# Kernel tuning notes

Hardware: AMD Instinct MI355X
Metric: run time of the kernel (lower is better)

The kernel has to match this reference:

```python
import jax, jax.numpy as jnp
import numpy as np

B = 65536
IN = 32 * 8      # input_size * n_dim
H = 256          # joint_hidden_size


def setup_inputs() -> dict:
    key = jax.random.key(0)
    ks = jax.random.split(key, 8)
    joint_h = jax.random.normal(ks[0], (B, H), dtype=jnp.float32)
    mgn_h = jax.random.normal(ks[1], (B, IN), dtype=jnp.float32)
    # xavier-uniform scale for W, plain normal for U (orthogonal in torch; any
    # dense matrix is fine for a numerical reference), zeros for biases.
    w_lim = float(np.sqrt(6.0 / (IN + H)))
    W_r = jax.random.uniform(ks[2], (IN, H), jnp.float32, -w_lim, w_lim)
    W_z = jax.random.uniform(ks[3], (IN, H), jnp.float32, -w_lim, w_lim)
    W_h = jax.random.uniform(ks[4], (IN, H), jnp.float32, -w_lim, w_lim)
    U_r = jax.random.normal(ks[5], (H, H), jnp.float32) / np.float32(np.sqrt(H))
    U_z = jax.random.normal(ks[6], (H, H), jnp.float32) / np.float32(np.sqrt(H))
    U_h = jax.random.normal(ks[7], (H, H), jnp.float32) / np.float32(np.sqrt(H))
    b_r = jnp.zeros((H,), jnp.float32)
    b_z = jnp.zeros((H,), jnp.float32)
    b_h = jnp.zeros((H,), jnp.float32)
    return {"joint_h": joint_h, "mgn_h": mgn_h,
            "W_r": W_r, "W_z": W_z, "W_h": W_h,
            "U_r": U_r, "U_z": U_z, "U_h": U_h,
            "b_r": b_r, "b_z": b_z, "b_h": b_h}


def reference(joint_h, mgn_h, W_r, W_z, W_h, U_r, U_z, U_h, b_r, b_z, b_h):
    # fuse the three input GEMMs and the two non-gated hidden GEMMs by
    # concatenating weights (same math as 6 separate mm's)
    W = jnp.concatenate([W_r, W_z, W_h], axis=1)        # [IN, 3H]
    U_rz = jnp.concatenate([U_r, U_z], axis=1)          # [H, 2H]
    x_proj = mgn_h @ W                                  # [B, 3H]
    h_proj = joint_h @ U_rz                             # [B, 2H]
    Hd = joint_h.shape[1]
    r = jax.nn.sigmoid(x_proj[:, :Hd] + h_proj[:, :Hd] + b_r)
    z = jax.nn.sigmoid(x_proj[:, Hd:2 * Hd] + h_proj[:, Hd:] + b_z)
    h_tilde = jnp.tanh(x_proj[:, 2 * Hd:] + (joint_h * r) @ U_h + b_h)
    return h_tilde + z * (joint_h - h_tilde)
```

## Files before the change

kernel.cpp:

```cpp
#include <hip/hip_runtime.h>

#define H     256
#define BM    128
#define NTHR  512
#define LDK2  264

typedef __attribute__((ext_vector_type(4)))  float f32x4;
typedef __attribute__((ext_vector_type(16))) float f32x16;
typedef __attribute__((ext_vector_type(8)))  short bf16x8;

__device__ __forceinline__ ushort f2bf(float f) {
    union { float f; unsigned u; } v; v.f = f;
    unsigned u = v.u;
    unsigned r = (u + 0x7fffu + ((u >> 16) & 1u)) >> 16;
    return (ushort)r;
}
__device__ __forceinline__ float bf2f(ushort h) {
    union { unsigned u; float f; } v; v.u = ((unsigned)h) << 16;
    return v.f;
}
__device__ __forceinline__ float sigmoid_f(float x) {
    return __builtin_amdgcn_rcpf(1.0f + __expf(-x));
}
__device__ __forceinline__ float tanh_f(float x) {
    float ax = fabsf(x);
    float e  = __expf(-2.0f * ax);
    float t  = (1.0f - e) * __builtin_amdgcn_rcpf(1.0f + e);
    return copysignf(t, x);
}

__global__ void prep_w(const float* __restrict__ Wr, const float* __restrict__ Wz,
                       const float* __restrict__ Wh, const float* __restrict__ Ur,
                       const float* __restrict__ Uz, const float* __restrict__ Uh,
                       ushort* __restrict__ P)
{
    const int k  = blockIdx.x;
    const int kk = k & 255;
    const bool hi = k >= 256;
    for (int n = threadIdx.x; n < 768; n += 256) {
        float v;
        if (n < 256)      v = (hi ? Ur : Wr)[kk * 256 + n];
        else if (n < 512) v = (hi ? Uz : Wz)[kk * 256 + (n - 256)];
        else              v = (hi ? Uh : Wh)[kk * 256 + (n - 512)];
        P[(size_t)n * 512 + k] = f2bf(v);
    }
}

#define MFMA32(a, b, c) __builtin_amdgcn_mfma_f32_32x32x16_bf16((a), (b), (c), 0, 0, 0)

#define LBRZ(B, BR, BZ) do {                                                  \
    const int ko_ = ((B) < 16) ? (B) * 16 : 256 + ((B) - 16) * 16;            \
    BR = *(const bf16x8*)(pBr + ko_);                                         \
    BZ = *(const bf16x8*)(pBz + ko_);                                         \
} while (0)

#define LBH(B, BH) do {                                                       \
    const int ko_ = ((B) < 16) ? 256 + (B) * 16 : ((B) - 16) * 16;            \
    BH = *(const bf16x8*)(pBh + ko_);                                         \
} while (0)

#define STEP1(SB, S16, BR, BZ) do {                                           \
    const int kk_ = (S16) * 16;                                               \
    bf16x8 af_[4];                                                            \
    _Pragma("unroll") for (int rf_ = 0; rf_ < 4; ++rf_)                       \
        af_[rf_] = *(const bf16x8*)&SB[(rf_ * 32 + l31) * LDK2 + kk_ + hi8];  \
    _Pragma("unroll") for (int rf_ = 0; rf_ < 4; ++rf_) {                     \
        aR[rf_] = MFMA32(af_[rf_], BR, aR[rf_]);                              \
        aZ[rf_] = MFMA32(af_[rf_], BZ, aZ[rf_]);                              \
    }                                                                         \
} while (0)

#define STEP2(SB, S16, BH) do {                                               \
    const int kk_ = (S16) * 16;                                               \
    bf16x8 af_[4];                                                            \
    _Pragma("unroll") for (int rf_ = 0; rf_ < 4; ++rf_)                       \
        af_[rf_] = *(const bf16x8*)&SB[(rf_ * 32 + l31) * LDK2 + kk_ + hi8];  \
    _Pragma("unroll") for (int rf_ = 0; rf_ < 4; ++rf_)                       \
        aH[rf_] = MFMA32(af_[rf_], BH, aH[rf_]);                              \
} while (0)

#define LOADJ(C) do {                                                         \
    _Pragma("unroll") for (int i_ = 0; i_ < 4; ++i_) {                        \
        const int c_ = tid + ((C) * 4 + i_) * NTHR;                           \
        jv[i_] = *(const f32x4*)(joint + (r0 + (c_ >> 6)) * H + (c_ & 63) * 4); \
    }                                                                         \
} while (0)

#define COMMITJ(C) do {                                                       \
    _Pragma("unroll") for (int i_ = 0; i_ < 4; ++i_) {                        \
        const int c_ = tid + ((C) * 4 + i_) * NTHR;                           \
        ushort4 w_;                                                           \
        w_.x = f2bf(jv[i_][0]); w_.y = f2bf(jv[i_][1]);                       \
        w_.z = f2bf(jv[i_][2]); w_.w = f2bf(jv[i_][3]);                       \
        *(ushort4*)&sb1[(c_ >> 6) * LDK2 + (c_ & 63) * 4] = w_;               \
    }                                                                         \
} while (0)

__global__ __launch_bounds__(NTHR, 2)
void gru_main(const float* __restrict__ joint, const float* __restrict__ mgn,
              const ushort* __restrict__ P,
              const float* __restrict__ br_, const float* __restrict__ bz_,
              const float* __restrict__ bh_, float* __restrict__ out)
{
    __shared__ ushort sb0[BM * LDK2];
    __shared__ ushort sb1[BM * LDK2];

    const int tid  = threadIdx.x;
    const int wave = tid >> 6;
    const int lane = tid & 63;
    const int l31  = lane & 31;
    const int hi8  = (lane >> 5) * 8;
    const int hi4  = (lane >> 5) * 4;
    const int colbase = wave * 32;
    const int col  = colbase + l31;
    const size_t r0 = (size_t)blockIdx.x * BM;

    const ushort* __restrict__ pBr = P + (size_t)col * 512 + hi8;
    const ushort* __restrict__ pBz = pBr + (size_t)256 * 512;
    const ushort* __restrict__ pBh = pBr + (size_t)512 * 512;

    #pragma unroll
    for (int b = 0; b < 2; ++b) {
        f32x4 mv[8];
        #pragma unroll
        for (int i = 0; i < 8; ++i) {
            const int c = tid + (b * 8 + i) * NTHR;
            mv[i] = *(const f32x4*)(mgn + (r0 + (c >> 6)) * H + (c & 63) * 4);
        }
        #pragma unroll
        for (int i = 0; i < 8; ++i) {
            const int c = tid + (b * 8 + i) * NTHR;
            ushort4 w;
            w.x = f2bf(mv[i][0]); w.y = f2bf(mv[i][1]);
            w.z = f2bf(mv[i][2]); w.w = f2bf(mv[i][3]);
            *(ushort4*)&sb0[(c >> 6) * LDK2 + (c & 63) * 4] = w;
        }
    }
    __syncthreads();

    f32x16 aR[4], aZ[4];
    #pragma unroll
    for (int rf = 0; rf < 4; ++rf)
        #pragma unroll
        for (int e = 0; e < 16; ++e) { aR[rf][e] = 0.f; aZ[rf][e] = 0.f; }

    {
        f32x4 jv[4];
        bf16x8 bRA, bZA, bRB, bZB, bRC, bZC, bRD, bZD;
        LBRZ(0, bRA, bZA); LBRZ(1, bRB, bZB); LBRZ(2, bRC, bZC); LBRZ(3, bRD, bZD);
        LOADJ(0);
        STEP1(sb0, 0, bRA, bZA);  LBRZ(4, bRA, bZA);
        STEP1(sb0, 1, bRB, bZB);  LBRZ(5, bRB, bZB);
        STEP1(sb0, 2, bRC, bZC);  LBRZ(6, bRC, bZC);
        COMMITJ(0); LOADJ(1);
        STEP1(sb0, 3, bRD, bZD);  LBRZ(7, bRD, bZD);
        STEP1(sb0, 4, bRA, bZA);  LBRZ(8, bRA, bZA);
        STEP1(sb0, 5, bRB, bZB);  LBRZ(9, bRB, bZB);
        COMMITJ(1); LOADJ(2);
        STEP1(sb0, 6, bRC, bZC);  LBRZ(10, bRC, bZC);
        STEP1(sb0, 7, bRD, bZD);  LBRZ(11, bRD, bZD);
        STEP1(sb0, 8, bRA, bZA);  LBRZ(12, bRA, bZA);
        COMMITJ(2); LOADJ(3);
        STEP1(sb0, 9, bRB, bZB);  LBRZ(13, bRB, bZB);
        STEP1(sb0, 10, bRC, bZC); LBRZ(14, bRC, bZC);
        STEP1(sb0, 11, bRD, bZD); LBRZ(15, bRD, bZD);
        COMMITJ(3);
        STEP1(sb0, 12, bRA, bZA); LBRZ(16, bRA, bZA);
        STEP1(sb0, 13, bRB, bZB); LBRZ(17, bRB, bZB);
        STEP1(sb0, 14, bRC, bZC); LBRZ(18, bRC, bZC);
        STEP1(sb0, 15, bRD, bZD); LBRZ(19, bRD, bZD);
        __syncthreads();
        STEP1(sb1, 0, bRA, bZA);  LBRZ(20, bRA, bZA);
        STEP1(sb1, 1, bRB, bZB);  LBRZ(21, bRB, bZB);
        STEP1(sb1, 2, bRC, bZC);  LBRZ(22, bRC, bZC);
        STEP1(sb1, 3, bRD, bZD);  LBRZ(23, bRD, bZD);
        STEP1(sb1, 4, bRA, bZA);  LBRZ(24, bRA, bZA);
        STEP1(sb1, 5, bRB, bZB);  LBRZ(25, bRB, bZB);
        STEP1(sb1, 6, bRC, bZC);  LBRZ(26, bRC, bZC);
        STEP1(sb1, 7, bRD, bZD);  LBRZ(27, bRD, bZD);
        STEP1(sb1, 8, bRA, bZA);  LBRZ(28, bRA, bZA);
        STEP1(sb1, 9, bRB, bZB);  LBRZ(29, bRB, bZB);
        STEP1(sb1, 10, bRC, bZC); LBRZ(30, bRC, bZC);
        STEP1(sb1, 11, bRD, bZD); LBRZ(31, bRD, bZD);
        STEP1(sb1, 12, bRA, bZA);
        STEP1(sb1, 13, bRB, bZB);
        STEP1(sb1, 14, bRC, bZC);
        STEP1(sb1, 15, bRD, bZD);
    }
    __syncthreads();

    bf16x8 bHA, bHB, bHC, bHD;
    LBH(0, bHA); LBH(1, bHB); LBH(2, bHC); LBH(3, bHD);

    uint hs[32], zs[32];
    {
        const float brv = br_[col];
        const float bzv = bz_[col];
        #pragma unroll
        for (int rf = 0; rf < 4; ++rf)
            #pragma unroll
            for (int m = 0; m < 16; m += 2) {
                ushort hb[2], zb[2];
                #pragma unroll
                for (int e = 0; e < 2; ++e) {
                    const int mm  = m + e;
                    const int row = rf * 32 + (mm & 3) + 8 * (mm >> 2) + hi4;
                    const int idx = row * LDK2 + col;
                    const float r = sigmoid_f(aR[rf][mm] + brv);
                    hb[e] = sb1[idx];
                    sb1[idx] = f2bf(bf2f(hb[e]) * r);
                    zb[e] = f2bf(sigmoid_f(aZ[rf][mm] + bzv));
                }
                hs[rf * 8 + (m >> 1)] = (uint)hb[0] | ((uint)hb[1] << 16);
                zs[rf * 8 + (m >> 1)] = (uint)zb[0] | ((uint)zb[1] << 16);
            }
    }
    __syncthreads();

    f32x16 aH[4];
    #pragma unroll
    for (int rf = 0; rf < 4; ++rf)
        #pragma unroll
        for (int e = 0; e < 16; ++e) aH[rf][e] = 0.f;

    {
        STEP2(sb1, 0, bHA);  LBH(4, bHA);
        STEP2(sb1, 1, bHB);  LBH(5, bHB);
        STEP2(sb1, 2, bHC);  LBH(6, bHC);
        STEP2(sb1, 3, bHD);  LBH(7, bHD);
        STEP2(sb1, 4, bHA);  LBH(8, bHA);
        STEP2(sb1, 5, bHB);  LBH(9, bHB);
        STEP2(sb1, 6, bHC);  LBH(10, bHC);
        STEP2(sb1, 7, bHD);  LBH(11, bHD);
        STEP2(sb1, 8, bHA);  LBH(12, bHA);
        STEP2(sb1, 9, bHB);  LBH(13, bHB);
        STEP2(sb1, 10, bHC); LBH(14, bHC);
        STEP2(sb1, 11, bHD); LBH(15, bHD);
        STEP2(sb1, 12, bHA); LBH(16, bHA);
        STEP2(sb1, 13, bHB); LBH(17, bHB);
        STEP2(sb1, 14, bHC); LBH(18, bHC);
        STEP2(sb1, 15, bHD); LBH(19, bHD);
        STEP2(sb0, 0, bHA);  LBH(20, bHA);
        STEP2(sb0, 1, bHB);  LBH(21, bHB);
        STEP2(sb0, 2, bHC);  LBH(22, bHC);
        STEP2(sb0, 3, bHD);  LBH(23, bHD);
        STEP2(sb0, 4, bHA);  LBH(24, bHA);
        STEP2(sb0, 5, bHB);  LBH(25, bHB);
        STEP2(sb0, 6, bHC);  LBH(26, bHC);
        STEP2(sb0, 7, bHD);  LBH(27, bHD);
        STEP2(sb0, 8, bHA);  LBH(28, bHA);
        STEP2(sb0, 9, bHB);  LBH(29, bHB);
        STEP2(sb0, 10, bHC); LBH(30, bHC);
        STEP2(sb0, 11, bHD); LBH(31, bHD);
        STEP2(sb0, 12, bHA);
        STEP2(sb0, 13, bHB);
        STEP2(sb0, 14, bHC);
        STEP2(sb0, 15, bHD);
    }

    {
        const float bhv = bh_[col];
        #pragma unroll
        for (int rf = 0; rf < 4; ++rf)
            #pragma unroll
            for (int m = 0; m < 16; ++m) {
                const int row = rf * 32 + (m & 3) + 8 * (m >> 2) + hi4;
                const float ht = tanh_f(aH[rf][m] + bhv);
                const uint pk  = hs[rf * 8 + (m >> 1)];
                const uint pz  = zs[rf * 8 + (m >> 1)];
                const float h  = bf2f((ushort)(pk >> ((m & 1) * 16)));
                const float z  = bf2f((ushort)(pz >> ((m & 1) * 16)));
                out[(r0 + row) * H + col] = ht + z * (h - ht);
            }
    }
}

extern "C" void kernel_launch(void* const* d_in, const int* in_sizes, int n_in,
                              void* d_out, int out_size, void* d_ws, size_t ws_size,
                              hipStream_t stream)
{
    const float* joint = (const float*)d_in[0];
    const float* mgn   = (const float*)d_in[1];
    const float* Wr    = (const float*)d_in[2];
    const float* Wz    = (const float*)d_in[3];
    const float* Wh    = (const float*)d_in[4];
    const float* Ur    = (const float*)d_in[5];
    const float* Uz    = (const float*)d_in[6];
    const float* Uh    = (const float*)d_in[7];
    const float* br    = (const float*)d_in[8];
    const float* bz    = (const float*)d_in[9];
    const float* bh    = (const float*)d_in[10];

    ushort* P  = (ushort*)d_ws;
    float* out = (float*)d_out;

    prep_w<<<512, 256, 0, stream>>>(Wr, Wz, Wh, Ur, Uz, Uh, P);

    const int nrows = 65536;
    gru_main<<<nrows / BM, NTHR, 0, stream>>>(joint, mgn, P, br, bz, bh, out);
}
```

Before: 93.55 us.

## Process two row tiles per block and prefetch next mgn tile during GEMM

Each block now handles two 128-row tiles instead of one, halving the grid. During the second half of the U_h GEMM on the first tile, it loads and converts the next tile's mgn rows into the freed shared buffer, then swaps buffers. The goal is to hide the initial global-load latency of the second tile and amortize bias loads and setup. The cost is fewer blocks, which may reduce parallelism with 256 blocks on the device. It also adds more register pressure from the extra prefetch. The bf16 conversion also switches to the library intrinsic.

```diff
diff --git a/kernel.cpp b/kernel.cpp
--- a/kernel.cpp
+++ b/kernel.cpp
@@ -1,4 +1,5 @@
 #include <hip/hip_runtime.h>
+#include <hip/hip_bf16.h>
 
 #define H     256
 #define BM    128
@@ -10,10 +11,9 @@
 typedef __attribute__((ext_vector_type(8)))  short bf16x8;
 
 __device__ __forceinline__ ushort f2bf(float f) {
-    union { float f; unsigned u; } v; v.f = f;
-    unsigned u = v.u;
-    unsigned r = (u + 0x7fffu + ((u >> 16) & 1u)) >> 16;
-    return (ushort)r;
+    union { __hip_bfloat16 b; ushort u; } v;
+    v.b = __float2bfloat16(f);
+    return v.u;
 }
 __device__ __forceinline__ float bf2f(ushort h) {
     union { unsigned u; float f; } v; v.u = ((unsigned)h) << 16;
@@ -92,7 +92,24 @@
         ushort4 w_;                                                           \
         w_.x = f2bf(jv[i_][0]); w_.y = f2bf(jv[i_][1]);                       \
         w_.z = f2bf(jv[i_][2]); w_.w = f2bf(jv[i_][3]);                       \
-        *(ushort4*)&sb1[(c_ >> 6) * LDK2 + (c_ & 63) * 4] = w_;               \
+        *(ushort4*)&sbJ[(c_ >> 6) * LDK2 + (c_ & 63) * 4] = w_;               \
+    }                                                                         \
+} while (0)
+
+#define LOADM2(C) do {                                                        \
+    _Pragma("unroll") for (int i_ = 0; i_ < 4; ++i_) {                        \
+        const int c_ = tid + ((C) * 4 + i_) * NTHR;                           \
+        mv[i_] = *(const f32x4*)(mgn + (r0 + BM + (c_ >> 6)) * H + (c_ & 63) * 4); \
+    }                                                                         \
+} while (0)
+
+#define COMMITM2(C) do {                                                      \
+    _Pragma("unroll") for (int i_ = 0; i_ < 4; ++i_) {                        \
+        const int c_ = tid + ((C) * 4 + i_) * NTHR;                           \
+        ushort4 w_;                                                           \
+        w_.x = f2bf(mv[i_][0]); w_.y = f2bf(mv[i_][1]);                       \
+        w_.z = f2bf(mv[i_][2]); w_.w = f2bf(mv[i_][3]);                       \
+        *(ushort4*)&sbJ[(c_ >> 6) * LDK2 + (c_ & 63) * 4] = w_;               \
     }                                                                         \
 } while (0)
 
@@ -102,8 +119,8 @@
               const float* __restrict__ br_, const float* __restrict__ bz_,
               const float* __restrict__ bh_, float* __restrict__ out)
 {
-    __shared__ ushort sb0[BM * LDK2];
-    __shared__ ushort sb1[BM * LDK2];
+    __shared__ ushort sbA[BM * LDK2];
+    __shared__ ushort sbB[BM * LDK2];
 
     const int tid  = threadIdx.x;
     const int wave = tid >> 6;
@@ -113,89 +130,79 @@
     const int hi4  = (lane >> 5) * 4;
     const int colbase = wave * 32;
     const int col  = colbase + l31;
-    const size_t r0 = (size_t)blockIdx.x * BM;
 
     const ushort* __restrict__ pBr = P + (size_t)col * 512 + hi8;
     const ushort* __restrict__ pBz = pBr + (size_t)256 * 512;
     const ushort* __restrict__ pBh = pBr + (size_t)512 * 512;
 
-    #pragma unroll
-    for (int b = 0; b < 2; ++b) {
-        f32x4 mv[8];
-        #pragma unroll
-        for (int i = 0; i < 8; ++i) {
-            const int c = tid + (b * 8 + i) * NTHR;
-            mv[i] = *(const f32x4*)(mgn + (r0 + (c >> 6)) * H + (c & 63) * 4);
-        }
-        #pragma unroll
-        for (int i = 0; i < 8; ++i) {
-            const int c = tid + (b * 8 + i) * NTHR;
-            ushort4 w;
-            w.x = f2bf(mv[i][0]); w.y = f2bf(mv[i][1]);
-            w.z = f2bf(mv[i][2]); w.w = f2bf(mv[i][3]);
-            *(ushort4*)&sb0[(c >> 6) * LDK2 + (c & 63) * 4] = w;
+    const float brv = br_[col];
+    const float bzv = bz_[col];
+    const float bhv = bh_[col];
+
+    {
+        const size_t rr = (size_t)blockIdx.x * (2 * BM);
+        #pragma unroll
+        for (int b = 0; b < 2; ++b) {
+            f32x4 v[8];
+            #pragma unroll
+            for (int i = 0; i < 8; ++i) {
+                const int c = tid + (b * 8 + i) * NTHR;
+                v[i] = *(const f32x4*)(mgn + (rr + (c >> 6)) * H + (c & 63) * 4);
+            }
+            #pragma unroll
+            for (int i = 0; i < 8; ++i) {
+                const int c = tid + (b * 8 + i) * NTHR;
+                ushort4 w;
+                w.x = f2bf(v[i][0]); w.y = f2bf(v[i][1]);
+                w.z = f2bf(v[i][2]); w.w = f2bf(v[i][3]);
+                *(ushort4*)&sbA[(c >> 6) * LDK2 + (c & 63) * 4] = w;
+            }
         }
     }
     __syncthreads();
 
-    f32x16 aR[4], aZ[4];
+    ushort* sbM = sbA;
+    ushort* sbJ = sbB;
+
     #pragma unroll
-    for (int rf = 0; rf < 4; ++rf)
-        #pragma unroll
-        for (int e = 0; e < 16; ++e) { aR[rf][e] = 0.f; aZ[rf][e] = 0.f; }
-
-    {
-        f32x4 jv[4];
-        bf16x8 bRA, bZA, bRB, bZB, bRC, bZC, bRD, bZD;
-        LBRZ(0, bRA, bZA); LBRZ(1, bRB, bZB); LBRZ(2, bRC, bZC); LBRZ(3, bRD, bZD);
-        LOADJ(0);
-        STEP1(sb0, 0, bRA, bZA);  LBRZ(4, bRA, bZA);
-        STEP1(sb0, 1, bRB, bZB);  LBRZ(5, bRB, bZB);
-        STEP1(sb0, 2, bRC, bZC);  LBRZ(6, bRC, bZC);
-        COMMITJ(0); LOADJ(1);
-        STEP1(sb0, 3, bRD, bZD);  LBRZ(7, bRD, bZD);
-        STEP1(sb0, 4, bRA, bZA);  LBRZ(8, bRA, bZA);
-        STEP1(sb0, 5, bRB, bZB);  LBRZ(9, bRB, bZB);
-        COMMITJ(1); LOADJ(2);
-        STEP1(sb0, 6, bRC, bZC);  LBRZ(10, bRC, bZC);
-        STEP1(sb0, 7, bRD, bZD);  LBRZ(11, bRD, bZD);
-        STEP1(sb0, 8, bRA, bZA);  LBRZ(12, bRA, bZA);
-        COMMITJ(2); LOADJ(3);
-        STEP1(sb0, 9, bRB, bZB);  LBRZ(13, bRB, bZB);
-        STEP1(sb0, 10, bRC, bZC); LBRZ(14, bRC, bZC);
-        STEP1(sb0, 11, bRD, bZD); LBRZ(15, bRD, bZD);
-        COMMITJ(3);
-        STEP1(sb0, 12, bRA, bZA); LBRZ(16, bRA, bZA);
-        STEP1(sb0, 13, bRB, bZB); LBRZ(17, bRB, bZB);
-        STEP1(sb0, 14, bRC, bZC); LBRZ(18, bRC, bZC);
-        STEP1(sb0, 15, bRD, bZD); LBRZ(19, bRD, bZD);
-        __syncthreads();
-        STEP1(sb1, 0, bRA, bZA);  LBRZ(20, bRA, bZA);
-        STEP1(sb1, 1, bRB, bZB);  LBRZ(21, bRB, bZB);
-        STEP1(sb1, 2, bRC, bZC);  LBRZ(22, bRC, bZC);
-        STEP1(sb1, 3, bRD, bZD);  LBRZ(23, bRD, bZD);
-        STEP1(sb1, 4, bRA, bZA);  LBRZ(24, bRA, bZA);
-        STEP1(sb1, 5, bRB, bZB);  LBRZ(25, bRB, bZB);
-        STEP1(sb1, 6, bRC, bZC);  LBRZ(26, bRC, bZC);
-        STEP1(sb1, 7, bRD, bZD);  LBRZ(27, bRD, bZD);
-        STEP1(sb1, 8, bRA, bZA);  LBRZ(28, bRA, bZA);
-        STEP1(sb1, 9, bRB, bZB);  LBRZ(29, bRB, bZB);
-        STEP1(sb1, 10, bRC, bZC); LBRZ(30, bRC, bZC);
-        STEP1(sb1, 11, bRD, bZD); LBRZ(31, bRD, bZD);
-        STEP1(sb1, 12, bRA, bZA);
-        STEP1(sb1, 13, bRB, bZB);
-        STEP1(sb1, 14, bRC, bZC);
-        STEP1(sb1, 15, bRD, bZD);
-    }
-    __syncthreads();
-
-    bf16x8 bHA, bHB, bHC, bHD;
-    LBH(0, bHA); LBH(1, bHB); LBH(2, bHC); LBH(3, bHD);
-
-    uint hs[32], zs[32];
-    {
-        const float brv = br_[col];
-        const float bzv = bz_[col];
+    for (int t = 0; t < 2; ++t) {
+        const size_t r0 = (size_t)blockIdx.x * (2 * BM) + (size_t)t * BM;
+
+        f32x16 aR[4], aZ[4];
+        #pragma unroll
+        for (int rf = 0; rf < 4; ++rf)
+            #pragma unroll
+            for (int e = 0; e < 16; ++e) { aR[rf][e] = 0.f; aZ[rf][e] = 0.f; }
+
+        {
+            f32x4 jv[4];
+            bf16x8 bR[4], bZ[4];
+            #pragma unroll
+            for (int s = 0; s < 4; ++s) LBRZ(s, bR[s], bZ[s]);
+            LOADJ(0);
+            #pragma unroll
+            for (int s = 0; s < 16; ++s) {
+                STEP1(sbM, s, bR[s & 3], bZ[s & 3]);
+                LBRZ(s + 4, bR[s & 3], bZ[s & 3]);
+                if (s == 2)       { COMMITJ(0); LOADJ(1); }
+                else if (s == 5)  { COMMITJ(1); LOADJ(2); }
+                else if (s == 8)  { COMMITJ(2); LOADJ(3); }
+                else if (s == 11) { COMMITJ(3); }
+            }
+            __syncthreads();
+            #pragma unroll
+            for (int s = 0; s < 16; ++s) {
+                STEP1(sbJ, s, bR[s & 3], bZ[s & 3]);
+                if (s < 12) LBRZ(s + 20, bR[s & 3], bZ[s & 3]);
+            }
+        }
+        __syncthreads();
+
+        bf16x8 bH[4];
+        #pragma unroll
+        for (int s = 0; s < 4; ++s) LBH(s, bH[s]);
+
+        uint hs[32], zs[32];
         #pragma unroll
         for (int rf = 0; rf < 4; ++rf)
             #pragma unroll
@@ -207,59 +214,44 @@
                     const int row = rf * 32 + (mm & 3) + 8 * (mm >> 2) + hi4;
                     const int idx = row * LDK2 + col;
                     const float r = sigmoid_f(aR[rf][mm] + brv);
-                    hb[e] = sb1[idx];
-                    sb1[idx] = f2bf(bf2f(hb[e]) * r);
+                    hb[e] = sbJ[idx];
+                    sbJ[idx] = f2bf(bf2f(hb[e]) * r);
                     zb[e] = f2bf(sigmoid_f(aZ[rf][mm] + bzv));
                 }
                 hs[rf * 8 + (m >> 1)] = (uint)hb[0] | ((uint)hb[1] << 16);
                 zs[rf * 8 + (m >> 1)] = (uint)zb[0] | ((uint)zb[1] << 16);
             }
-    }
-    __syncthreads();
-
-    f32x16 aH[4];
-    #pragma unroll
-    for (int rf = 0; rf < 4; ++rf)
-        #pragma unroll
-        for (int e = 0; e < 16; ++e) aH[rf][e] = 0.f;
-
-    {
-        STEP2(sb1, 0, bHA);  LBH(4, bHA);
-        STEP2(sb1, 1, bHB);  LBH(5, bHB);
-        STEP2(sb1, 2, bHC);  LBH(6, bHC);
-        STEP2(sb1, 3, bHD);  LBH(7, bHD);
-        STEP2(sb1, 4, bHA);  LBH(8, bHA);
-        STEP2(sb1, 5, bHB);  LBH(9, bHB);
-        STEP2(sb1, 6, bHC);  LBH(10, bHC);
-        STEP2(sb1, 7, bHD);  LBH(11, bHD);
-        STEP2(sb1, 8, bHA);  LBH(12, bHA);
-        STEP2(sb1, 9, bHB);  LBH(13, bHB);
-        STEP2(sb1, 10, bHC); LBH(14, bHC);
-        STEP2(sb1, 11, bHD); LBH(15, bHD);
-        STEP2(sb1, 12, bHA); LBH(16, bHA);
-        STEP2(sb1, 13, bHB); LBH(17, bHB);
-        STEP2(sb1, 14, bHC); LBH(18, bHC);
-        STEP2(sb1, 15, bHD); LBH(19, bHD);
-        STEP2(sb0, 0, bHA);  LBH(20, bHA);
-        STEP2(sb0, 1, bHB);  LBH(21, bHB);
-        STEP2(sb0, 2, bHC);  LBH(22, bHC);
-        STEP2(sb0, 3, bHD);  LBH(23, bHD);
-        STEP2(sb0, 4, bHA);  LBH(24, bHA);
-        STEP2(sb0, 5, bHB);  LBH(25, bHB);
-        STEP2(sb0, 6, bHC);  LBH(26, bHC);
-        STEP2(sb0, 7, bHD);  LBH(27, bHD);
-        STEP2(sb0, 8, bHA);  LBH(28, bHA);
-        STEP2(sb0, 9, bHB);  LBH(29, bHB);
-        STEP2(sb0, 10, bHC); LBH(30, bHC);
-        STEP2(sb0, 11, bHD); LBH(31, bHD);
-        STEP2(sb0, 12, bHA);
-        STEP2(sb0, 13, bHB);
-        STEP2(sb0, 14, bHC);
-        STEP2(sb0, 15, bHD);
-    }
-
-    {
-        const float bhv = bh_[col];
+        __syncthreads();
+
+        f32x16 aH[4];
+        #pragma unroll
+        for (int rf = 0; rf < 4; ++rf)
+            #pragma unroll
+            for (int e = 0; e < 16; ++e) aH[rf][e] = 0.f;
+
+        #pragma unroll
+        for (int s = 0; s < 16; ++s) {
+            STEP2(sbJ, s, bH[s & 3]);
+            LBH(s + 4, bH[s & 3]);
+        }
+        __syncthreads();
+
+        {
+            f32x4 mv[4];
+            #pragma unroll
+            for (int s = 0; s < 16; ++s) {
+                STEP2(sbM, s, bH[s & 3]);
+                if (s < 12) LBH(s + 20, bH[s & 3]);
+                if (t == 0) {
+                    if (s == 0)       { LOADM2(0); }
+                    else if (s == 2)  { COMMITM2(0); LOADM2(1); }
+                    else if (s == 5)  { COMMITM2(1); LOADM2(2); }
+                    else if (s == 8)  { COMMITM2(2); LOADM2(3); }
+                    else if (s == 11) { COMMITM2(3); }
+                }
+            }
+        }
+
         #pragma unroll
         for (int rf = 0; rf < 4; ++rf)
             #pragma unroll
@@ -272,6 +264,9 @@
                 const float z  = bf2f((ushort)(pz >> ((m & 1) * 16)));
                 out[(r0 + row) * H + col] = ht + z * (h - ht);
             }
+
+        __syncthreads();
+        ushort* tmp = sbM; sbM = sbJ; sbJ = tmp;
     }
 }
 
@@ -297,5 +292,5 @@
     prep_w<<<512, 256, 0, stream>>>(Wr, Wz, Wh, Ur, Uz, Uh, P);
 
     const int nrows = 65536;
-    gru_main<<<nrows / BM, NTHR, 0, stream>>>(joint, mgn, P, br, bz, bh, out);
-}
+    gru_main<<<nrows / (2 * BM), NTHR, 0, stream>>>(joint, mgn, P, br, bz, bh, out);
+}
```

New measurement: 161.6 us. 1.73x slower.

## Retile waves to 64x64 output blocks and use hardware bf16 conversion

Applied to the files above, without the earlier changes.

Each wave now covers a 64-row by 64-column output tile (2x2 MFMA fragments) instead of 128 rows by 32 columns. This halves the LDS A-fragment reads per MFMA, at the cost of doubling the per-wave global B-fragment loads from the weight matrix. The bf16 conversion switches from manual rounding to the __float2bfloat16 intrinsic, which may map to a hardware conversion instruction. The B prefetch schedule is reduced from four buffers to two in the first GEMM, which shortens the latency-hiding distance for weight loads.

```diff
diff --git a/kernel.cpp b/kernel.cpp
--- a/kernel.cpp
+++ b/kernel.cpp
@@ -1,4 +1,5 @@
 #include <hip/hip_runtime.h>
+#include <hip/hip_bf16.h>
 
 #define H     256
 #define BM    128
@@ -10,10 +11,9 @@
 typedef __attribute__((ext_vector_type(8)))  short bf16x8;
 
 __device__ __forceinline__ ushort f2bf(float f) {
-    union { float f; unsigned u; } v; v.f = f;
-    unsigned u = v.u;
-    unsigned r = (u + 0x7fffu + ((u >> 16) & 1u)) >> 16;
-    return (ushort)r;
+    union { __hip_bfloat16 b; ushort u; } v;
+    v.b = __float2bfloat16(f);
+    return v.u;
 }
 __device__ __forceinline__ float bf2f(ushort h) {
     union { unsigned u; float f; } v; v.u = ((unsigned)h) << 16;
@@ -48,35 +48,42 @@
 
 #define MFMA32(a, b, c) __builtin_amdgcn_mfma_f32_32x32x16_bf16((a), (b), (c), 0, 0, 0)
 
-#define LBRZ(B, BR, BZ) do {                                                  \
+#define LBRZ(B, R0, R1, Z0, Z1) do {                                          \
     const int ko_ = ((B) < 16) ? (B) * 16 : 256 + ((B) - 16) * 16;            \
-    BR = *(const bf16x8*)(pBr + ko_);                                         \
-    BZ = *(const bf16x8*)(pBz + ko_);                                         \
-} while (0)
-
-#define LBH(B, BH) do {                                                       \
+    R0 = *(const bf16x8*)(pBr + ko_);                                         \
+    R1 = *(const bf16x8*)(pBr + (size_t)32 * 512 + ko_);                      \
+    Z0 = *(const bf16x8*)(pBz + ko_);                                         \
+    Z1 = *(const bf16x8*)(pBz + (size_t)32 * 512 + ko_);                      \
+} while (0)
+
+#define LBH(B, H0, H1) do {                                                   \
     const int ko_ = ((B) < 16) ? 256 + (B) * 16 : ((B) - 16) * 16;            \
-    BH = *(const bf16x8*)(pBh + ko_);                                         \
-} while (0)
-
-#define STEP1(SB, S16, BR, BZ) do {                                           \
+    H0 = *(const bf16x8*)(pBh + ko_);                                         \
+    H1 = *(const bf16x8*)(pBh + (size_t)32 * 512 + ko_);                      \
+} while (0)
+
+#define STEP1(SB, S16, R0, R1, Z0, Z1) do {                                   \
     const int kk_ = (S16) * 16;                                               \
-    bf16x8 af_[4];                                                            \
-    _Pragma("unroll") for (int rf_ = 0; rf_ < 4; ++rf_)                       \
-        af_[rf_] = *(const bf16x8*)&SB[(rf_ * 32 + l31) * LDK2 + kk_ + hi8];  \
-    _Pragma("unroll") for (int rf_ = 0; rf_ < 4; ++rf_) {                     \
-        aR[rf_] = MFMA32(af_[rf_], BR, aR[rf_]);                              \
-        aZ[rf_] = MFMA32(af_[rf_], BZ, aZ[rf_]);                              \
-    }                                                                         \
-} while (0)
-
-#define STEP2(SB, S16, BH) do {                                               \
+    bf16x8 a0_ = *(const bf16x8*)&SB[(rowbase + l31) * LDK2 + kk_ + hi8];     \
+    bf16x8 a1_ = *(const bf16x8*)&SB[(rowbase + 32 + l31) * LDK2 + kk_ + hi8];\
+    aR[0][0] = MFMA32(a0_, R0, aR[0][0]);                                     \
+    aR[1][0] = MFMA32(a1_, R0, aR[1][0]);                                     \
+    aZ[0][0] = MFMA32(a0_, Z0, aZ[0][0]);                                     \
+    aZ[1][0] = MFMA32(a1_, Z0, aZ[1][0]);                                     \
+    aR[0][1] = MFMA32(a0_, R1, aR[0][1]);                                     \
+    aR[1][1] = MFMA32(a1_, R1, aR[1][1]);                                     \
+    aZ[0][1] = MFMA32(a0_, Z1, aZ[0][1]);                                     \
+    aZ[1][1] = MFMA32(a1_, Z1, aZ[1][1]);                                     \
+} while (0)
+
+#define STEP2(SB, S16, H0, H1) do {                                           \
     const int kk_ = (S16) * 16;                                               \
-    bf16x8 af_[4];                                                            \
-    _Pragma("unroll") for (int rf_ = 0; rf_ < 4; ++rf_)                       \
-        af_[rf_] = *(const bf16x8*)&SB[(rf_ * 32 + l31) * LDK2 + kk_ + hi8];  \
-    _Pragma("unroll") for (int rf_ = 0; rf_ < 4; ++rf_)                       \
-        aH[rf_] = MFMA32(af_[rf_], BH, aH[rf_]);                              \
+    bf16x8 a0_ = *(const bf16x8*)&SB[(rowbase + l31) * LDK2 + kk_ + hi8];     \
+    bf16x8 a1_ = *(const bf16x8*)&SB[(rowbase + 32 + l31) * LDK2 + kk_ + hi8];\
+    aH[0][0] = MFMA32(a0_, H0, aH[0][0]);                                     \
+    aH[1][0] = MFMA32(a1_, H0, aH[1][0]);                                     \
+    aH[0][1] = MFMA32(a0_, H1, aH[0][1]);                                     \
+    aH[1][1] = MFMA32(a1_, H1, aH[1][1]);                                     \
 } while (0)
 
 #define LOADJ(C) do {                                                         \
@@ -111,11 +118,11 @@
     const int l31  = lane & 31;
     const int hi8  = (lane >> 5) * 8;
     const int hi4  = (lane >> 5) * 4;
-    const int colbase = wave * 32;
-    const int col  = colbase + l31;
+    const int rowbase = (wave >> 2) * 64;
+    const int colb    = (wave & 3) * 64;
     const size_t r0 = (size_t)blockIdx.x * BM;
 
-    const ushort* __restrict__ pBr = P + (size_t)col * 512 + hi8;
+    const ushort* __restrict__ pBr = P + (size_t)(colb + l31) * 512 + hi8;
     const ushort* __restrict__ pBz = pBr + (size_t)256 * 512;
     const ushort* __restrict__ pBh = pBr + (size_t)512 * 512;
 
@@ -138,139 +145,152 @@
     }
     __syncthreads();
 
-    f32x16 aR[4], aZ[4];
+    f32x16 aR[2][2], aZ[2][2];
     #pragma unroll
-    for (int rf = 0; rf < 4; ++rf)
-        #pragma unroll
-        for (int e = 0; e < 16; ++e) { aR[rf][e] = 0.f; aZ[rf][e] = 0.f; }
+    for (int rf = 0; rf < 2; ++rf)
+        #pragma unroll
+        for (int cf = 0; cf < 2; ++cf)
+            #pragma unroll
+            for (int e = 0; e < 16; ++e) { aR[rf][cf][e] = 0.f; aZ[rf][cf][e] = 0.f; }
 
     {
         f32x4 jv[4];
-        bf16x8 bRA, bZA, bRB, bZB, bRC, bZC, bRD, bZD;
-        LBRZ(0, bRA, bZA); LBRZ(1, bRB, bZB); LBRZ(2, bRC, bZC); LBRZ(3, bRD, bZD);
+        bf16x8 rA0, rA1, zA0, zA1, rB0, rB1, zB0, zB1;
+        LBRZ(0, rA0, rA1, zA0, zA1);
+        LBRZ(1, rB0, rB1, zB0, zB1);
         LOADJ(0);
-        STEP1(sb0, 0, bRA, bZA);  LBRZ(4, bRA, bZA);
-        STEP1(sb0, 1, bRB, bZB);  LBRZ(5, bRB, bZB);
-        STEP1(sb0, 2, bRC, bZC);  LBRZ(6, bRC, bZC);
+        STEP1(sb0, 0, rA0, rA1, zA0, zA1);  LBRZ(2, rA0, rA1, zA0, zA1);
+        STEP1(sb0, 1, rB0, rB1, zB0, zB1);  LBRZ(3, rB0, rB1, zB0, zB1);
+        STEP1(sb0, 2, rA0, rA1, zA0, zA1);  LBRZ(4, rA0, rA1, zA0, zA1);
         COMMITJ(0); LOADJ(1);
-        STEP1(sb0, 3, bRD, bZD);  LBRZ(7, bRD, bZD);
-        STEP1(sb0, 4, bRA, bZA);  LBRZ(8, bRA, bZA);
-        STEP1(sb0, 5, bRB, bZB);  LBRZ(9, bRB, bZB);
+        STEP1(sb0, 3, rB0, rB1, zB0, zB1);  LBRZ(5, rB0, rB1, zB0, zB1);
+        STEP1(sb0, 4, rA0, rA1, zA0, zA1);  LBRZ(6, rA0, rA1, zA0, zA1);
+        STEP1(sb0, 5, rB0, rB1, zB0, zB1);  LBRZ(7, rB0, rB1, zB0, zB1);
         COMMITJ(1); LOADJ(2);
-        STEP1(sb0, 6, bRC, bZC);  LBRZ(10, bRC, bZC);
-        STEP1(sb0, 7, bRD, bZD);  LBRZ(11, bRD, bZD);
-        STEP1(sb0, 8, bRA, bZA);  LBRZ(12, bRA, bZA);
+        STEP1(sb0, 6, rA0, rA1, zA0, zA1);  LBRZ(8, rA0, rA1, zA0, zA1);
+        STEP1(sb0, 7, rB0, rB1, zB0, zB1);  LBRZ(9, rB0, rB1, zB0, zB1);
+        STEP1(sb0, 8, rA0, rA1, zA0, zA1);  LBRZ(10, rA0, rA1, zA0, zA1);
         COMMITJ(2); LOADJ(3);
-        STEP1(sb0, 9, bRB, bZB);  LBRZ(13, bRB, bZB);
-        STEP1(sb0, 10, bRC, bZC); LBRZ(14, bRC, bZC);
-        STEP1(sb0, 11, bRD, bZD); LBRZ(15, bRD, bZD);
+        STEP1(sb0, 9, rB0, rB1, zB0, zB1);  LBRZ(11, rB0, rB1, zB0, zB1);
+        STEP1(sb0, 10, rA0, rA1, zA0, zA1); LBRZ(12, rA0, rA1, zA0, zA1);
+        STEP1(sb0, 11, rB0, rB1, zB0, zB1); LBRZ(13, rB0, rB1, zB0, zB1);
         COMMITJ(3);
-        STEP1(sb0, 12, bRA, bZA); LBRZ(16, bRA, bZA);
-        STEP1(sb0, 13, bRB, bZB); LBRZ(17, bRB, bZB);
-        STEP1(sb0, 14, bRC, bZC); LBRZ(18, bRC, bZC);
-        STEP1(sb0, 15, bRD, bZD); LBRZ(19, bRD, bZD);
+        STEP1(sb0, 12, rA0, rA1, zA0, zA1); LBRZ(14, rA0, rA1, zA0, zA1);
+        STEP1(sb0, 13, rB0, rB1, zB0, zB1); LBRZ(15, rB0, rB1, zB0, zB1);
+        STEP1(sb0, 14, rA0, rA1, zA0, zA1); LBRZ(16, rA0, rA1, zA0, zA1);
+        STEP1(sb0, 15, rB0, rB1, zB0, zB1); LBRZ(17, rB0, rB1, zB0, zB1);
         __syncthreads();
-        STEP1(sb1, 0, bRA, bZA);  LBRZ(20, bRA, bZA);
-        STEP1(sb1, 1, bRB, bZB);  LBRZ(21, bRB, bZB);
-        STEP1(sb1, 2, bRC, bZC);  LBRZ(22, bRC, bZC);
-        STEP1(sb1, 3, bRD, bZD);  LBRZ(23, bRD, bZD);
-        STEP1(sb1, 4, bRA, bZA);  LBRZ(24, bRA, bZA);
-        STEP1(sb1, 5, bRB, bZB);  LBRZ(25, bRB, bZB);
-        STEP1(sb1, 6, bRC, bZC);  LBRZ(26, bRC, bZC);
-        STEP1(sb1, 7, bRD, bZD);  LBRZ(27, bRD, bZD);
-        STEP1(sb1, 8, bRA, bZA);  LBRZ(28, bRA, bZA);
-        STEP1(sb1, 9, bRB, bZB);  LBRZ(29, bRB, bZB);
-        STEP1(sb1, 10, bRC, bZC); LBRZ(30, bRC, bZC);
-        STEP1(sb1, 11, bRD, bZD); LBRZ(31, bRD, bZD);
-        STEP1(sb1, 12, bRA, bZA);
-        STEP1(sb1, 13, bRB, bZB);
-        STEP1(sb1, 14, bRC, bZC);
-        STEP1(sb1, 15, bRD, bZD);
+        STEP1(sb1, 0, rA0, rA1, zA0, zA1);  LBRZ(18, rA0, rA1, zA0, zA1);
+        STEP1(sb1, 1, rB0, rB1, zB0, zB1);  LBRZ(19, rB0, rB1, zB0, zB1);
+        STEP1(sb1, 2, rA0, rA1, zA0, zA1);  LBRZ(20, rA0, rA1, zA0, zA1);
+        STEP1(sb1, 3, rB0, rB1, zB0, zB1);  LBRZ(21, rB0, rB1, zB0, zB1);
+        STEP1(sb1, 4, rA0, rA1, zA0, zA1);  LBRZ(22, rA0, rA1, zA0, zA1);
+        STEP1(sb1, 5, rB0, rB1, zB0, zB1);  LBRZ(23, rB0, rB1, zB0, zB1);
+        STEP1(sb1, 6, rA0, rA1, zA0, zA1);  LBRZ(24, rA0, rA1, zA0, zA1);
+        STEP1(sb1, 7, rB0, rB1, zB0, zB1);  LBRZ(25, rB0, rB1, zB0, zB1);
+        STEP1(sb1, 8, rA0, rA1, zA0, zA1);  LBRZ(26, rA0, rA1, zA0, zA1);
+        STEP1(sb1, 9, rB0, rB1, zB0, zB1);  LBRZ(27, rB0, rB1, zB0, zB1);
+        STEP1(sb1, 10, rA0, rA1, zA0, zA1); LBRZ(28, rA0, rA1, zA0, zA1);
+        STEP1(sb1, 11, rB0, rB1, zB0, zB1); LBRZ(29, rB0, rB1, zB0, zB1);
+        STEP1(sb1, 12, rA0, rA1, zA0, zA1); LBRZ(30, rA0, rA1, zA0, zA1);
+        STEP1(sb1, 13, rB0, rB1, zB0, zB1); LBRZ(31, rB0, rB1, zB0, zB1);
+        STEP1(sb1, 14, rA0, rA1, zA0, zA1);
+        STEP1(sb1, 15, rB0, rB1, zB0, zB1);
     }
     __syncthreads();
 
-    bf16x8 bHA, bHB, bHC, bHD;
-    LBH(0, bHA); LBH(1, bHB); LBH(2, bHC); LBH(3, bHD);
+    bf16x8 hA0, hA1, hB0, hB1, hC0, hC1, hD0, hD1;
+    LBH(0, hA0, hA1); LBH(1, hB0, hB1); LBH(2, hC0, hC1); LBH(3, hD0, hD1);
 
     uint hs[32], zs[32];
     {
-        const float brv = br_[col];
-        const float bzv = bz_[col];
-        #pragma unroll
-        for (int rf = 0; rf < 4; ++rf)
+        #pragma unroll
+        for (int rf = 0; rf < 2; ++rf)
             #pragma unroll
-            for (int m = 0; m < 16; m += 2) {
-                ushort hb[2], zb[2];
+            for (int cf = 0; cf < 2; ++cf) {
+                const int c   = colb + cf * 32 + l31;
+                const float brv = br_[c];
+                const float bzv = bz_[c];
                 #pragma unroll
-                for (int e = 0; e < 2; ++e) {
-                    const int mm  = m + e;
-                    const int row = rf * 32 + (mm & 3) + 8 * (mm >> 2) + hi4;
-                    const int idx = row * LDK2 + col;
-                    const float r = sigmoid_f(aR[rf][mm] + brv);
-                    hb[e] = sb1[idx];
-                    sb1[idx] = f2bf(bf2f(hb[e]) * r);
-                    zb[e] = f2bf(sigmoid_f(aZ[rf][mm] + bzv));
+                for (int m = 0; m < 16; m += 2) {
+                    ushort hb[2], zb[2];
+                    #pragma unroll
+                    for (int e = 0; e < 2; ++e) {
+                        const int mm  = m + e;
+                        const int row = rowbase + rf * 32 + (mm & 3) + 8 * (mm >> 2) + hi4;
+                        const int idx = row * LDK2 + c;
+                        const float r = sigmoid_f(aR[rf][cf][mm] + brv);
+                        hb[e] = sb1[idx];
+                        sb1[idx] = f2bf(bf2f(hb[e]) * r);
+                        zb[e] = f2bf(sigmoid_f(aZ[rf][cf][mm] + bzv));
+                    }
+                    hs[(rf * 2 + cf) * 8 + (m >> 1)] = (uint)hb[0] | ((uint)hb[1] << 16);
+                    zs[(rf * 2 + cf) * 8 + (m >> 1)] = (uint)zb[0] | ((uint)zb[1] << 16);
                 }
-                hs[rf * 8 + (m >> 1)] = (uint)hb[0] | ((uint)hb[1] << 16);
-                zs[rf * 8 + (m >> 1)] = (uint)zb[0] | ((uint)zb[1] << 16);
             }
     }
     __syncthreads();
 
-    f32x16 aH[4];
+    f32x16 aH[2][2];
     #pragma unroll
-    for (int rf = 0; rf < 4; ++rf)
-        #pragma unroll
-        for (int e = 0; e < 16; ++e) aH[rf][e] = 0.f;
+    for (int rf = 0; rf < 2; ++rf)
+        #pragma unroll
+        for (int cf = 0; cf < 2; ++cf)
+            #pragma unroll
+            for (int e = 0; e < 16; ++e) aH[rf][cf][e] = 0.f;
 
     {
-        STEP2(sb1, 0, bHA);  LBH(4, bHA);
-        STEP2(sb1, 1, bHB);  LBH(5, bHB);
-        STEP2(sb1, 2, bHC);  LBH(6, bHC);
-        STEP2(sb1, 3, bHD);  LBH(7, bHD);
-        STEP2(sb1, 4, bHA);  LBH(8, bHA);
-        STEP2(sb1, 5, bHB);  LBH(9, bHB);
-        STEP2(sb1, 6, bHC);  LBH(10, bHC);
-        STEP2(sb1, 7, bHD);  LBH(11, bHD);
-        STEP2(sb1, 8, bHA);  LBH(12, bHA);
-        STEP2(sb1, 9, bHB);  LBH(13, bHB);
-        STEP2(sb1, 10, bHC); LBH(14, bHC);
-        STEP2(sb1, 11, bHD); LBH(15, bHD);
-        STEP2(sb1, 12, bHA); LBH(16, bHA);
-        STEP2(sb1, 13, bHB); LBH(17, bHB);
-        STEP2(sb1, 14, bHC); LBH(18, bHC);
-        STEP2(sb1, 15, bHD); LBH(19, bHD);
-        STEP2(sb0, 0, bHA);  LBH(20, bHA);
-        STEP2(sb0, 1, bHB);  LBH(21, bHB);
-        STEP2(sb0, 2, bHC);  LBH(22, bHC);
-        STEP2(sb0, 3, bHD);  LBH(23, bHD);
-        STEP2(sb0, 4, bHA);  LBH(24, bHA);
-        STEP2(sb0, 5, bHB);  LBH(25, bHB);
-        STEP2(sb0, 6, bHC);  LBH(26, bHC);
-        STEP2(sb0, 7, bHD);  LBH(27, bHD);
-        STEP2(sb0, 8, bHA);  LBH(28, bHA);
-        STEP2(sb0, 9, bHB);  LBH(29, bHB);
-        STEP2(sb0, 10, bHC); LBH(30, bHC);
-        STEP2(sb0, 11, bHD); LBH(31, bHD);
-        STEP2(sb0, 12, bHA);
-        STEP2(sb0, 13, bHB);
-        STEP2(sb0, 14, bHC);
-        STEP2(sb0, 15, bHD);
+        STEP2(sb1, 0, hA0, hA1);  LBH(4, hA0, hA1);
+        STEP2(sb1, 1, hB0, hB1);  LBH(5, hB0, hB1);
+        STEP2(sb1, 2, hC0, hC1);  LBH(6, hC0, hC1);
+        STEP2(sb1, 3, hD0, hD1);  LBH(7, hD0, hD1);
+        STEP2(sb1, 4, hA0, hA1);  LBH(8, hA0, hA1);
+        STEP2(sb1, 5, hB0, hB1);  LBH(9, hB0, hB1);
+        STEP2(sb1, 6, hC0, hC1);  LBH(10, hC0, hC1);
+        STEP2(sb1, 7, hD0, hD1);  LBH(11, hD0, hD1);
+        STEP2(sb1, 8, hA0, hA1);  LBH(12, hA0, hA1);
+        STEP2(sb1, 9, hB0, hB1);  LBH(13, hB0, hB1);
+        STEP2(sb1, 10, hC0, hC1); LBH(14, hC0, hC1);
+        STEP2(sb1, 11, hD0, hD1); LBH(15, hD0, hD1);
+        STEP2(sb1, 12, hA0, hA1); LBH(16, hA0, hA1);
+        STEP2(sb1, 13, hB0, hB1); LBH(17, hB0, hB1);
+        STEP2(sb1, 14, hC0, hC1); LBH(18, hC0, hC1);
+        STEP2(sb1, 15, hD0, hD1); LBH(19, hD0, hD1);
+        STEP2(sb0, 0, hA0, hA1);  LBH(20, hA0, hA1);
+        STEP2(sb0, 1, hB0, hB1);  LBH(21, hB0, hB1);
+        STEP2(sb0, 2, hC0, hC1);  LBH(22, hC0, hC1);
+        STEP2(sb0, 3, hD0, hD1);  LBH(23, hD0, hD1);
+        STEP2(sb0, 4, hA0, hA1);  LBH(24, hA0, hA1);
+        STEP2(sb0, 5, hB0, hB1);  LBH(25, hB0, hB1);
+        STEP2(sb0, 6, hC0, hC1);  LBH(26, hC0, hC1);
+        STEP2(sb0, 7, hD0, hD1);  LBH(27, hD0, hD1);
+        STEP2(sb0, 8, hA0, hA1);  LBH(28, hA0, hA1);
+        STEP2(sb0, 9, hB0, hB1);  LBH(29, hB0, hB1);
+        STEP2(sb0, 10, hC0, hC1); LBH(30, hC0, hC1);
+        STEP2(sb0, 11, hD0, hD1); LBH(31, hD0, hD1);
+        STEP2(sb0, 12, hA0, hA1);
+        STEP2(sb0, 13, hB0, hB1);
+        STEP2(sb0, 14, hC0, hC1);
+        STEP2(sb0, 15, hD0, hD1);
     }
 
     {
-        const float bhv = bh_[col];
-        #pragma unroll
-        for (int rf = 0; rf < 4; ++rf)
+        #pragma unroll
+        for (int rf = 0; rf < 2; ++rf)
             #pragma unroll
-            for (int m = 0; m < 16; ++m) {
-                const int row = rf * 32 + (m & 3) + 8 * (m >> 2) + hi4;
-                const float ht = tanh_f(aH[rf][m] + bhv);
-                const uint pk  = hs[rf * 8 + (m >> 1)];
-                const uint pz  = zs[rf * 8 + (m >> 1)];
-                const float h  = bf2f((ushort)(pk >> ((m & 1) * 16)));
-                const float z  = bf2f((ushort)(pz >> ((m & 1) * 16)));
-                out[(r0 + row) * H + col] = ht + z * (h - ht);
+            for (int cf = 0; cf < 2; ++cf) {
+                const int c = colb + cf * 32 + l31;
+                const float bhv = bh_[c];
+                #pragma unroll
+                for (int m = 0; m < 16; ++m) {
+                    const int row = rowbase + rf * 32 + (m & 3) + 8 * (m >> 2) + hi4;
+                    const float ht = tanh_f(aH[rf][cf][m] + bhv);
+                    const uint pk  = hs[(rf * 2 + cf) * 8 + (m >> 1)];
+                    const uint pz  = zs[(rf * 2 + cf) * 8 + (m >> 1)];
+                    const float h  = bf2f((ushort)(pk >> ((m & 1) * 16)));
+                    const float z  = bf2f((ushort)(pz >> ((m & 1) * 16)));
+                    out[(r0 + row) * H + c] = ht + z * (h - ht);
+                }
             }
     }
 }
```

Result: slower. 134.8 us (+44.0%).
